# Performance work log

Measured on AMD Instinct MI355X. Metric: run time of the kernel, lower is better.

Reference implementation:

```python
import jax, jax.numpy as jnp
import numpy as np

B, N, E, D, AD = 8, 1000, 4, 64, 32  # batch, n_node, n_edge_types, state_dim, annotation_dim
W_SCALE = 0.02  # matches normal_(0.0, 0.02) init


def setup_inputs() -> dict:
    key = jax.random.key(0)
    ks = jax.random.split(key, 10)
    return {
        "prop_state": jax.random.normal(ks[0], (B, N, D), jnp.float32),
        "annotation": jax.random.normal(ks[1], (B, N, AD), jnp.float32),
        "A": jax.random.uniform(ks[2], (B, N, 2 * N * E), jnp.float32),
        "W_in": W_SCALE * jax.random.normal(ks[3], (E, D, D), jnp.float32),
        "W_out": W_SCALE * jax.random.normal(ks[4], (E, D, D), jnp.float32),
        "W_r": W_SCALE * jax.random.normal(ks[5], (D, 3 * D), jnp.float32),
        "W_z": W_SCALE * jax.random.normal(ks[6], (D, 3 * D), jnp.float32),
        "W_h": W_SCALE * jax.random.normal(ks[7], (D, 3 * D), jnp.float32),
        "Wo1": W_SCALE * jax.random.normal(ks[8], (D, D + AD), jnp.float32),
        "Wo2": W_SCALE * jax.random.normal(ks[9], (1, D), jnp.float32),
    }


def _propagate(state, A_in, A_out, W_in, W_out, W_r, W_z, W_h):
    b, n, d = state.shape
    e = W_in.shape[0]
    # per-edge-type linear transforms (torch Linear: y = x @ W.T), batched over edge types
    # layout matches torch: stack over e then transpose(0,1) -> [b, e, n, d] -> [b, e*n, d]
    s_in = jnp.einsum('bnd,efd->benf', state, W_in).reshape(b, e * n, d)
    s_out = jnp.einsum('bnd,efd->benf', state, W_out).reshape(b, e * n, d)
    a_in = jnp.matmul(A_in, s_in)    # [b, n, d]
    a_out = jnp.matmul(A_out, s_out)  # [b, n, d]
    a = jnp.concatenate([a_in, a_out, state], axis=2)  # [b, n, 3d]
    r = jax.nn.sigmoid(a @ W_r.T)
    z = jax.nn.sigmoid(a @ W_z.T)
    joined = jnp.concatenate([a_in, a_out, r * state], axis=2)
    h_hat = jnp.tanh(joined @ W_h.T)
    return (1.0 - z) * state + z * h_hat


def reference(prop_state, annotation, A, W_in, W_out, W_r, W_z, W_h, Wo1, Wo2):
    n = prop_state.shape[1]
    e = W_in.shape[0]
    ne = n * e
    A_in, A_out = A[:, :, :ne], A[:, :, ne:]
    # exactly two propagation steps (n_steps_flag path in the original)
    s1 = _propagate(prop_state, A_in, A_out, W_in, W_out, W_r, W_z, W_h)
    s2 = _propagate(s1, A_in, A_out, W_in, W_out, W_r, W_z, W_h)
    join_state = jnp.concatenate([s2, annotation], axis=2)  # [b, n, d+ad]
    out = jnp.tanh(join_state @ Wo1.T) @ Wo2.T  # [b, n, 1]
    return out.sum(axis=2)  # [b, n]
```

## Files before the change

### kernel.cpp

```cpp
#include <hip/hip_runtime.h>


typedef float  f32x4_t  __attribute__((ext_vector_type(4)));
typedef __bf16 bf16x8_t __attribute__((ext_vector_type(8)));
typedef __bf16 bf16x4_t __attribute__((ext_vector_type(4)));

#define MFMA16(a, b, c) __builtin_amdgcn_mfma_f32_16x16x32_bf16((a), (b), (c), 0, 0, 0)

static constexpr int kN     = 1000;
static constexpr int kD     = 64;
static constexpr int kAD    = 32;
static constexpr int kNE    = 4000;
static constexpr int kSteps = 125;
static constexpr int kP     = 8000 * 64;

__device__ __forceinline__ float4 ld4(const float* p) {
    return *reinterpret_cast<const float4*>(p);
}

__device__ __forceinline__ bf16x8_t cvt8(float4 a, float4 b) {
    bf16x8_t r;
    r[0] = (__bf16)a.x; r[1] = (__bf16)a.y; r[2] = (__bf16)a.z; r[3] = (__bf16)a.w;
    r[4] = (__bf16)b.x; r[5] = (__bf16)b.y; r[6] = (__bf16)b.z; r[7] = (__bf16)b.w;
    return r;
}

__device__ __forceinline__ bf16x8_t sum4p(const float* p) {
    float s0 = 0.f, s1 = 0.f, s2 = 0.f, s3 = 0.f;
    float s4 = 0.f, s5 = 0.f, s6 = 0.f, s7 = 0.f;
    #pragma unroll
    for (int pl = 0; pl < 4; ++pl) {
        const float4 a0 = ld4(p + (size_t)pl * kP);
        const float4 a1 = ld4(p + (size_t)pl * kP + 4);
        s0 += a0.x; s1 += a0.y; s2 += a0.z; s3 += a0.w;
        s4 += a1.x; s5 += a1.y; s6 += a1.z; s7 += a1.w;
    }
    bf16x8_t r;
    r[0] = (__bf16)s0; r[1] = (__bf16)s1; r[2] = (__bf16)s2; r[3] = (__bf16)s3;
    r[4] = (__bf16)s4; r[5] = (__bf16)s5; r[6] = (__bf16)s6; r[7] = (__bf16)s7;
    return r;
}

__device__ __forceinline__ float sigm(float x) {
    x = fminf(fmaxf(x, -30.f), 30.f);
    return 1.0f / (1.0f + __expf(-x));
}

__device__ __forceinline__ float fast_tanh(float x) {
    x = fminf(fmaxf(x, -15.f), 15.f);
    const float e = __expf(-2.0f * x);
    return (1.0f - e) / (1.0f + e);
}

__global__ __launch_bounds__(256, 4) void relayout_A(
    const float* __restrict__ A, __bf16* __restrict__ Afrag)
{
    const int bx   = blockIdx.x;
    const int tile = bx & 15;
    const int rest = bx >> 4;
    const int kseg = rest % 5;
    const int rhb  = rest / 5;
    const int h    = rhb & 1;
    const int b    = rhb >> 1;

    const int t    = threadIdx.x;
    const int wv   = t >> 6;
    const int lane = t & 63;
    const int m    = lane & 15;
    const int q    = lane >> 4;

    __shared__ float L[64][133];

    const float* Abase = A + (size_t)b * kN * 8000 + h * 4000;
    const int sbase = kseg * 25;

    for (int kc = 0; kc < 800; kc += 128) {
        const int cw  = (kc < 768) ? 128 : 32;
        const int shl = (kc < 768) ? 5 : 3;
        const int rounds = (kc < 768) ? 8 : 2;
        const int kabs = kseg * 800 + kc;
        for (int p = 0; p < rounds; ++p) {
            const int idx = p * 256 + t;
            const int r   = idx >> shl;
            const int c4  = idx & ((cw >> 2) - 1);
            int i = tile * 64 + r;
            if (i >= kN) i = kN - 1;
            const float4 v = ld4(Abase + (size_t)i * 8000 + kabs + c4 * 4);
            *reinterpret_cast<float4*>(&L[r][c4 * 4]) = v;
        }
        __syncthreads();
        const int nst = cw >> 5;
        for (int sp = 0; sp < nst; ++sp) {
            const float4 a0 = *reinterpret_cast<const float4*>(&L[wv * 16 + m][sp * 32 + q * 8]);
            const float4 a1 = *reinterpret_cast<const float4*>(&L[wv * 16 + m][sp * 32 + q * 8 + 4]);
            const int s = sbase + (kc >> 5) + sp;
            const size_t el = ((((size_t)((b * 2 + h) * 64 + tile * 4 + wv)) * 125 + s) * 64 + lane) * 8;
            *reinterpret_cast<bf16x8_t*>(Afrag + el) = cvt8(a0, a1);
        }
        __syncthreads();
    }
}

__global__ __launch_bounds__(256) void precompute_swt(
    const float* __restrict__ state,
    const float* __restrict__ W_in,
    const float* __restrict__ W_out,
    __bf16* __restrict__ SWTfrag)
{
    const int bx = blockIdx.x;
    const int jt = bx & 15;
    const int e  = (bx >> 4) & 3;
    const int h  = (bx >> 6) & 1;
    const int b  = bx >> 7;
    const float* W = (h ? W_out : W_in) + e * kD * kD;

    const int tid  = threadIdx.x;
    const int w    = tid >> 6;
    const int lane = tid & 63;
    const int m    = lane & 15;
    const int q    = lane >> 4;

    __shared__ __bf16 T[64][72];

    const int  jj    = jt * 64 + w * 16 + m;
    const bool valid = (jj < kN);
    const float* srow = state + ((size_t)b * kN + (valid ? jj : kN - 1)) * kD + q * 8;
    float4 a0 = ld4(srow),      a1 = ld4(srow + 4);
    float4 a2 = ld4(srow + 32), a3 = ld4(srow + 36);
    if (!valid) {
        a0 = make_float4(0.f, 0.f, 0.f, 0.f); a1 = a0; a2 = a0; a3 = a0;
    }
    const bf16x8_t af0 = cvt8(a0, a1);
    const bf16x8_t af1 = cvt8(a2, a3);

    #pragma unroll
    for (int c = 0; c < 4; ++c) {
        const int f = c * 16 + m;
        const float* wrow = W + f * kD + q * 8;
        const bf16x8_t bf0 = cvt8(ld4(wrow),      ld4(wrow + 4));
        const bf16x8_t bf1 = cvt8(ld4(wrow + 32), ld4(wrow + 36));
        f32x4_t acc = {0.f, 0.f, 0.f, 0.f};
        acc = MFMA16(af0, bf0, acc);
        acc = MFMA16(af1, bf1, acc);
        const int j0 = w * 16 + q * 4;
        bf16x4_t v;
        v[0] = (__bf16)acc[0]; v[1] = (__bf16)acc[1];
        v[2] = (__bf16)acc[2]; v[3] = (__bf16)acc[3];
        *reinterpret_cast<bf16x4_t*>(&T[f][j0]) = v;
    }
    __syncthreads();

    const int bh = b * 2 + h;
    #pragma unroll
    for (int rep = 0; rep < 2; ++rep) {
        const int m2 = tid & 15;
        const int cc = (tid >> 4) & 3;
        const int ol = (tid >> 6) + rep * 4;
        const int j0 = jt * 64 + ol * 8;
        if (j0 < kN) {
            const int jg = e * kN + j0;
            const int s  = jg >> 5;
            const int qq = (jg >> 3) & 3;
            const uint4 v = *reinterpret_cast<uint4*>(&T[cc * 16 + m2][ol * 8]);
            const size_t el = ((((size_t)bh * 125 + s) * 4 + cc) * 64 + qq * 16 + m2) * 8;
            *reinterpret_cast<uint4*>((__bf16*)SWTfrag + el) = v;
        }
    }
}

__global__ __launch_bounds__(256, 4) void big_mm_f(
    const __bf16* __restrict__ Afrag,
    const __bf16* __restrict__ SWTfrag,
    float* __restrict__ a_in_p,
    float* __restrict__ a_out_p)
{
    const int bx   = blockIdx.x;
    const int tile = bx & 15;
    const int h    = (bx >> 4) & 1;
    const int b    = (bx >> 5) & 7;
    const int ksp  = bx >> 8;
    const int t    = threadIdx.x;
    const int wv   = t >> 6;
    const int lane = t & 63;
    const int m    = lane & 15;
    const int q    = lane >> 4;

    const int s0   = ksp * 32;
    const int send = (s0 + 32 < kSteps) ? s0 + 32 : kSteps;
    const int ns   = send - s0;

    const int bh = b * 2 + h;
    const __bf16* pA = Afrag +
        ((((size_t)(bh * 64 + tile * 4 + wv)) * 125 + s0) * 64 + lane) * 8;
    const __bf16* pB = SWTfrag +
        (((size_t)bh * 125 + s0) * 4 * 64) * 8 + (size_t)lane * 8;

    f32x4_t acc0 = {0.f, 0.f, 0.f, 0.f};
    f32x4_t acc1 = {0.f, 0.f, 0.f, 0.f};
    f32x4_t acc2 = {0.f, 0.f, 0.f, 0.f};
    f32x4_t acc3 = {0.f, 0.f, 0.f, 0.f};

    bf16x8_t cA  = *(const bf16x8_t*)(pA);
    bf16x8_t cB0 = *(const bf16x8_t*)(pB);
    bf16x8_t cB1 = *(const bf16x8_t*)(pB + 512);
    bf16x8_t cB2 = *(const bf16x8_t*)(pB + 1024);
    bf16x8_t cB3 = *(const bf16x8_t*)(pB + 1536);

    for (int s = 0; s < ns; ++s) {
        const int adv = (s + 1 < ns) ? 1 : 0;
        pA += adv * 512;
        pB += adv * 2048;
        const bf16x8_t nA  = *(const bf16x8_t*)(pA);
        const bf16x8_t nB0 = *(const bf16x8_t*)(pB);
        const bf16x8_t nB1 = *(const bf16x8_t*)(pB + 512);
        const bf16x8_t nB2 = *(const bf16x8_t*)(pB + 1024);
        const bf16x8_t nB3 = *(const bf16x8_t*)(pB + 1536);

        acc0 = MFMA16(cA, cB0, acc0);
        acc1 = MFMA16(cA, cB1, acc1);
        acc2 = MFMA16(cA, cB2, acc2);
        acc3 = MFMA16(cA, cB3, acc3);

        cA = nA; cB0 = nB0; cB1 = nB1; cB2 = nB2; cB3 = nB3;
    }

    float* dst = (h ? a_out_p : a_in_p) + (size_t)ksp * kP + (size_t)b * kN * kD;
    const int i0 = tile * 64 + wv * 16 + q * 4;
    #pragma unroll
    for (int r = 0; r < 4; ++r) {
        const int i = i0 + r;
        if (i < kN) {
            float* drow = dst + (size_t)i * kD + m;
            drow[0]  = acc0[r];
            drow[16] = acc1[r];
            drow[32] = acc2[r];
            drow[48] = acc3[r];
        }
    }
}

__global__ __launch_bounds__(256, 2) void gating(
    const float* __restrict__ a_in_p,
    const float* __restrict__ a_out_p,
    const float* __restrict__ state,
    const float* __restrict__ W_r,
    const float* __restrict__ W_z,
    const float* __restrict__ W_h,
    float* __restrict__ s_next,
    const float* __restrict__ ann,
    const float* __restrict__ Wo1,
    const float* __restrict__ Wo2,
    float* __restrict__ out,
    const int step)
{
    const int i0   = blockIdx.x * 16;
    const int tid  = threadIdx.x;
    const int c    = tid >> 6;
    const int lane = tid & 63;
    const int m    = lane & 15;
    const int q    = lane >> 4;
    const int f    = c * 16 + m;

    __shared__ __bf16 TL[16][72];
    __shared__ float  Osum[4][16];

    const size_t rowA = (size_t)(i0 + m);

    bf16x8_t xf[6];
    {
        const float* p = a_in_p + rowA * kD + q * 8;
        xf[0] = sum4p(p);
        xf[1] = sum4p(p + 32);
        p = a_out_p + rowA * kD + q * 8;
        xf[2] = sum4p(p);
        xf[3] = sum4p(p + 32);
        p = state + rowA * kD + q * 8;
        xf[4] = cvt8(ld4(p),      ld4(p + 4));
        xf[5] = cvt8(ld4(p + 32), ld4(p + 36));
    }

    f32x4_t accr = {0.f, 0.f, 0.f, 0.f};
    f32x4_t accz = {0.f, 0.f, 0.f, 0.f};
    f32x4_t acch = {0.f, 0.f, 0.f, 0.f};

    const float* wr = W_r + f * 192 + q * 8;
    const float* wz = W_z + f * 192 + q * 8;
    const float* wh = W_h + f * 192 + q * 8;
    #pragma unroll
    for (int kc = 0; kc < 6; ++kc) {
        accr = MFMA16(xf[kc], cvt8(ld4(wr + kc * 32), ld4(wr + kc * 32 + 4)), accr);
        accz = MFMA16(xf[kc], cvt8(ld4(wz + kc * 32), ld4(wz + kc * 32 + 4)), accz);
        if (kc < 4)
            acch = MFMA16(xf[kc], cvt8(ld4(wh + kc * 32), ld4(wh + kc * 32 + 4)), acch);
    }

    float sC[4];
    #pragma unroll
    for (int r = 0; r < 4; ++r)
        sC[r] = state[(size_t)(i0 + q * 4 + r) * kD + f];

    #pragma unroll
    for (int r = 0; r < 4; ++r)
        TL[q * 4 + r][f] = (__bf16)(sigm(accr[r]) * sC[r]);
    __syncthreads();
    const bf16x8_t rs0 = *(const bf16x8_t*)&TL[m][q * 8];
    const bf16x8_t rs1 = *(const bf16x8_t*)&TL[m][32 + q * 8];

    const float* wh3 = W_h + f * 192 + 128 + q * 8;
    acch = MFMA16(rs0, cvt8(ld4(wh3),      ld4(wh3 + 4)),  acch);
    acch = MFMA16(rs1, cvt8(ld4(wh3 + 32), ld4(wh3 + 36)), acch);

    float ns[4];
    #pragma unroll
    for (int r = 0; r < 4; ++r) {
        const float zv = sigm(accz[r]);
        ns[r] = (1.f - zv) * sC[r] + zv * fast_tanh(acch[r]);
    }

    if (step == 1) {
        #pragma unroll
        for (int r = 0; r < 4; ++r)
            s_next[(size_t)(i0 + q * 4 + r) * kD + f] = ns[r];
    } else {
        __syncthreads();
        #pragma unroll
        for (int r = 0; r < 4; ++r)
            TL[q * 4 + r][f] = (__bf16)ns[r];
        __syncthreads();
        const bf16x8_t j0 = *(const bf16x8_t*)&TL[m][q * 8];
        const bf16x8_t j1 = *(const bf16x8_t*)&TL[m][32 + q * 8];
        const float* ap = ann + rowA * kAD + q * 8;
        const bf16x8_t j2 = cvt8(ld4(ap), ld4(ap + 4));

        f32x4_t acco = {0.f, 0.f, 0.f, 0.f};
        const float* wo = Wo1 + (size_t)f * 96 + q * 8;
        acco = MFMA16(j0, cvt8(ld4(wo),      ld4(wo + 4)),  acco);
        acco = MFMA16(j1, cvt8(ld4(wo + 32), ld4(wo + 36)), acco);
        acco = MFMA16(j2, cvt8(ld4(wo + 64), ld4(wo + 68)), acco);

        const float w2 = Wo2[f];
        float vs[4];
        #pragma unroll
        for (int r = 0; r < 4; ++r)
            vs[r] = fast_tanh(acco[r]) * w2;
        #pragma unroll
        for (int off = 1; off <= 8; off <<= 1) {
            #pragma unroll
            for (int r = 0; r < 4; ++r)
                vs[r] += __shfl_xor(vs[r], off, 64);
        }
        if (m == 0) {
            #pragma unroll
            for (int r = 0; r < 4; ++r)
                Osum[c][q * 4 + r] = vs[r];
        }
        __syncthreads();
        if (tid < 16)
            out[i0 + tid] = Osum[0][tid] + Osum[1][tid] + Osum[2][tid] + Osum[3][tid];
    }
}

extern "C" void kernel_launch(void* const* d_in, const int* in_sizes, int n_in,
                              void* d_out, int out_size, void* d_ws, size_t ws_size,
                              hipStream_t stream) {
    (void)in_sizes; (void)n_in; (void)out_size; (void)ws_size;

    const float* prop_state = (const float*)d_in[0];
    const float* annotation = (const float*)d_in[1];
    const float* A          = (const float*)d_in[2];
    const float* W_in       = (const float*)d_in[3];
    const float* W_out      = (const float*)d_in[4];
    const float* W_r        = (const float*)d_in[5];
    const float* W_z        = (const float*)d_in[6];
    const float* W_h        = (const float*)d_in[7];
    const float* Wo1        = (const float*)d_in[8];
    const float* Wo2        = (const float*)d_in[9];
    float* out = (float*)d_out;

    char* ws = (char*)d_ws;
    __bf16* Afrag   = (__bf16*)(ws);
    __bf16* SWTfrag = (__bf16*)(ws + 131072000);
    float*  a_in_p  = (float*)(ws + 139264000);
    float*  a_out_p = (float*)(ws + 147456000);
    float*  s1      = (float*)(ws + 155648000);

    relayout_A<<<1280, 256, 0, stream>>>(A, Afrag);

    precompute_swt<<<1024, 256, 0, stream>>>(prop_state, W_in, W_out, SWTfrag);
    big_mm_f<<<1024, 256, 0, stream>>>(Afrag, SWTfrag, a_in_p, a_out_p);
    gating<<<500, 256, 0, stream>>>(a_in_p, a_out_p, prop_state, W_r, W_z, W_h,
                                    s1, nullptr, nullptr, nullptr, nullptr, 1);
    precompute_swt<<<1024, 256, 0, stream>>>(s1, W_in, W_out, SWTfrag);
    big_mm_f<<<1024, 256, 0, stream>>>(Afrag, SWTfrag, a_in_p, a_out_p);
    gating<<<500, 256, 0, stream>>>(a_in_p, a_out_p, s1, W_r, W_z, W_h,
                                    nullptr, annotation, Wo1, Wo2, out, 2);
}
```

Before: 516.1 us.

## Fuse A relayout into first propagation matmul and split K into five segments

Removes the standalone relayout kernel and folds it into a new fused_mm1 kernel. That kernel reads fp32 A, converts it to bf16 in shared memory, writes the fragment layout for reuse in step two, and runs the first-step MFMA directly from the staged tile. The second-step matmul and the gating reductions change from four 32-step K partitions to five 25-step partitions so both steps match, and the workspace offsets for the partial buffers grow to fit. This saves one full pass of reading the fp32 A tensor, at the cost of a heavier first matmul and one extra partial slice to store and sum.

```diff
diff --git a/kernel.cpp b/kernel.cpp
--- a/kernel.cpp
+++ b/kernel.cpp
@@ -10,9 +10,8 @@
 static constexpr int kN     = 1000;
 static constexpr int kD     = 64;
 static constexpr int kAD    = 32;
-static constexpr int kNE    = 4000;
-static constexpr int kSteps = 125;
 static constexpr int kP     = 8000 * 64;
+static constexpr int kPl    = 5;
 
 __device__ __forceinline__ float4 ld4(const float* p) {
     return *reinterpret_cast<const float4*>(p);
@@ -25,11 +24,11 @@
     return r;
 }
 
-__device__ __forceinline__ bf16x8_t sum4p(const float* p) {
+__device__ __forceinline__ bf16x8_t sum5p(const float* p) {
     float s0 = 0.f, s1 = 0.f, s2 = 0.f, s3 = 0.f;
     float s4 = 0.f, s5 = 0.f, s6 = 0.f, s7 = 0.f;
     #pragma unroll
-    for (int pl = 0; pl < 4; ++pl) {
+    for (int pl = 0; pl < kPl; ++pl) {
         const float4 a0 = ld4(p + (size_t)pl * kP);
         const float4 a1 = ld4(p + (size_t)pl * kP + 4);
         s0 += a0.x; s1 += a0.y; s2 += a0.z; s3 += a0.w;
@@ -50,55 +49,6 @@
     x = fminf(fmaxf(x, -15.f), 15.f);
     const float e = __expf(-2.0f * x);
     return (1.0f - e) / (1.0f + e);
-}
-
-__global__ __launch_bounds__(256, 4) void relayout_A(
-    const float* __restrict__ A, __bf16* __restrict__ Afrag)
-{
-    const int bx   = blockIdx.x;
-    const int tile = bx & 15;
-    const int rest = bx >> 4;
-    const int kseg = rest % 5;
-    const int rhb  = rest / 5;
-    const int h    = rhb & 1;
-    const int b    = rhb >> 1;
-
-    const int t    = threadIdx.x;
-    const int wv   = t >> 6;
-    const int lane = t & 63;
-    const int m    = lane & 15;
-    const int q    = lane >> 4;
-
-    __shared__ float L[64][133];
-
-    const float* Abase = A + (size_t)b * kN * 8000 + h * 4000;
-    const int sbase = kseg * 25;
-
-    for (int kc = 0; kc < 800; kc += 128) {
-        const int cw  = (kc < 768) ? 128 : 32;
-        const int shl = (kc < 768) ? 5 : 3;
-        const int rounds = (kc < 768) ? 8 : 2;
-        const int kabs = kseg * 800 + kc;
-        for (int p = 0; p < rounds; ++p) {
-            const int idx = p * 256 + t;
-            const int r   = idx >> shl;
-            const int c4  = idx & ((cw >> 2) - 1);
-            int i = tile * 64 + r;
-            if (i >= kN) i = kN - 1;
-            const float4 v = ld4(Abase + (size_t)i * 8000 + kabs + c4 * 4);
-            *reinterpret_cast<float4*>(&L[r][c4 * 4]) = v;
-        }
-        __syncthreads();
-        const int nst = cw >> 5;
-        for (int sp = 0; sp < nst; ++sp) {
-            const float4 a0 = *reinterpret_cast<const float4*>(&L[wv * 16 + m][sp * 32 + q * 8]);
-            const float4 a1 = *reinterpret_cast<const float4*>(&L[wv * 16 + m][sp * 32 + q * 8 + 4]);
-            const int s = sbase + (kc >> 5) + sp;
-            const size_t el = ((((size_t)((b * 2 + h) * 64 + tile * 4 + wv)) * 125 + s) * 64 + lane) * 8;
-            *reinterpret_cast<bf16x8_t*>(Afrag + el) = cvt8(a0, a1);
-        }
-        __syncthreads();
-    }
 }
 
 __global__ __launch_bounds__(256) void precompute_swt(
@@ -164,6 +114,101 @@
             const uint4 v = *reinterpret_cast<uint4*>(&T[cc * 16 + m2][ol * 8]);
             const size_t el = ((((size_t)bh * 125 + s) * 4 + cc) * 64 + qq * 16 + m2) * 8;
             *reinterpret_cast<uint4*>((__bf16*)SWTfrag + el) = v;
+        }
+    }
+}
+
+__global__ __launch_bounds__(256, 4) void fused_mm1(
+    const float* __restrict__ A,
+    const __bf16* __restrict__ SWTfrag,
+    __bf16* __restrict__ Afrag,
+    float* __restrict__ a_in_p,
+    float* __restrict__ a_out_p)
+{
+    const int bx   = blockIdx.x;
+    const int tile = bx & 15;
+    const int rest = bx >> 4;
+    const int kseg = rest % 5;
+    const int rhb  = rest / 5;
+    const int h    = rhb & 1;
+    const int b    = rhb >> 1;
+
+    const int t    = threadIdx.x;
+    const int wv   = t >> 6;
+    const int lane = t & 63;
+    const int m    = lane & 15;
+    const int q    = lane >> 4;
+
+    __shared__ __bf16 L[64][136];
+
+    const float* Abase = A + (size_t)b * kN * 8000 + h * 4000;
+    const int bh = b * 2 + h;
+
+    f32x4_t acc0 = {0.f, 0.f, 0.f, 0.f};
+    f32x4_t acc1 = {0.f, 0.f, 0.f, 0.f};
+    f32x4_t acc2 = {0.f, 0.f, 0.f, 0.f};
+    f32x4_t acc3 = {0.f, 0.f, 0.f, 0.f};
+
+    const __bf16* pBbase = SWTfrag + (size_t)bh * 125 * 2048 + (size_t)lane * 8;
+    __bf16* pAout = Afrag +
+        ((((size_t)(bh * 64 + tile * 4 + wv)) * 125) * 64 + lane) * 8;
+
+    for (int kc = 0; kc < 800; kc += 128) {
+        const int cw   = (kc < 768) ? 128 : 32;
+        const int kabs = kseg * 800 + kc;
+        if (cw == 128) {
+            #pragma unroll
+            for (int p = 0; p < 4; ++p) {
+                const int idx = p * 256 + t;
+                const int r   = idx >> 4;
+                const int c8  = idx & 15;
+                int i = tile * 64 + r;
+                if (i >= kN) i = kN - 1;
+                const float* src = Abase + (size_t)i * 8000 + kabs + c8 * 8;
+                *reinterpret_cast<bf16x8_t*>(&L[r][c8 * 8]) =
+                    cvt8(ld4(src), ld4(src + 4));
+            }
+        } else {
+            const int r  = t >> 2;
+            const int c8 = t & 3;
+            int i = tile * 64 + r;
+            if (i >= kN) i = kN - 1;
+            const float* src = Abase + (size_t)i * 8000 + kabs + c8 * 8;
+            *reinterpret_cast<bf16x8_t*>(&L[r][c8 * 8]) =
+                cvt8(ld4(src), ld4(src + 4));
+        }
+        __syncthreads();
+        const int nst = cw >> 5;
+        for (int sp = 0; sp < nst; ++sp) {
+            const int s = kseg * 25 + (kc >> 5) + sp;
+            const bf16x8_t af =
+                *reinterpret_cast<const bf16x8_t*>(&L[wv * 16 + m][sp * 32 + q * 8]);
+            *reinterpret_cast<bf16x8_t*>(pAout + (size_t)s * 512) = af;
+
+            const __bf16* pB = pBbase + (size_t)s * 2048;
+            const bf16x8_t b0 = *(const bf16x8_t*)(pB);
+            const bf16x8_t b1 = *(const bf16x8_t*)(pB + 512);
+            const bf16x8_t b2 = *(const bf16x8_t*)(pB + 1024);
+            const bf16x8_t b3 = *(const bf16x8_t*)(pB + 1536);
+            acc0 = MFMA16(af, b0, acc0);
+            acc1 = MFMA16(af, b1, acc1);
+            acc2 = MFMA16(af, b2, acc2);
+            acc3 = MFMA16(af, b3, acc3);
+        }
+        __syncthreads();
+    }
+
+    float* dst = (h ? a_out_p : a_in_p) + (size_t)kseg * kP + (size_t)b * kN * kD;
+    const int i0 = tile * 64 + wv * 16 + q * 4;
+    #pragma unroll
+    for (int r = 0; r < 4; ++r) {
+        const int i = i0 + r;
+        if (i < kN) {
+            float* drow = dst + (size_t)i * kD + m;
+            drow[0]  = acc0[r];
+            drow[16] = acc1[r];
+            drow[32] = acc2[r];
+            drow[48] = acc3[r];
         }
     }
 }
@@ -185,9 +230,8 @@
     const int m    = lane & 15;
     const int q    = lane >> 4;
 
-    const int s0   = ksp * 32;
-    const int send = (s0 + 32 < kSteps) ? s0 + 32 : kSteps;
-    const int ns   = send - s0;
+    const int s0 = ksp * 25;
+    const int ns = 25;
 
     const int bh = b * 2 + h;
     const __bf16* pA = Afrag +
@@ -269,11 +313,11 @@
     bf16x8_t xf[6];
     {
         const float* p = a_in_p + rowA * kD + q * 8;
-        xf[0] = sum4p(p);
-        xf[1] = sum4p(p + 32);
+        xf[0] = sum5p(p);
+        xf[1] = sum5p(p + 32);
         p = a_out_p + rowA * kD + q * 8;
-        xf[2] = sum4p(p);
-        xf[3] = sum4p(p + 32);
+        xf[2] = sum5p(p);
+        xf[3] = sum5p(p + 32);
         p = state + rowA * kD + q * 8;
         xf[4] = cvt8(ld4(p),      ld4(p + 4));
         xf[5] = cvt8(ld4(p + 32), ld4(p + 36));
@@ -381,17 +425,15 @@
     __bf16* Afrag   = (__bf16*)(ws);
     __bf16* SWTfrag = (__bf16*)(ws + 131072000);
     float*  a_in_p  = (float*)(ws + 139264000);
-    float*  a_out_p = (float*)(ws + 147456000);
-    float*  s1      = (float*)(ws + 155648000);
-
-    relayout_A<<<1280, 256, 0, stream>>>(A, Afrag);
+    float*  a_out_p = (float*)(ws + 149504000);
+    float*  s1      = (float*)(ws + 159744000);
 
     precompute_swt<<<1024, 256, 0, stream>>>(prop_state, W_in, W_out, SWTfrag);
-    big_mm_f<<<1024, 256, 0, stream>>>(Afrag, SWTfrag, a_in_p, a_out_p);
+    fused_mm1<<<1280, 256, 0, stream>>>(A, SWTfrag, Afrag, a_in_p, a_out_p);
     gating<<<500, 256, 0, stream>>>(a_in_p, a_out_p, prop_state, W_r, W_z, W_h,
                                     s1, nullptr, nullptr, nullptr, nullptr, 1);
     precompute_swt<<<1024, 256, 0, stream>>>(s1, W_in, W_out, SWTfrag);
-    big_mm_f<<<1024, 256, 0, stream>>>(Afrag, SWTfrag, a_in_p, a_out_p);
+    big_mm_f<<<1280, 256, 0, stream>>>(Afrag, SWTfrag, a_in_p, a_out_p);
     gating<<<500, 256, 0, stream>>>(a_in_p, a_out_p, s1, W_r, W_z, W_h,
                                     nullptr, annotation, Wo1, Wo2, out, 2);
 }
```

Result: faster. 498.0 us (-3.5%).
